# Kernel tuning notes

Hardware: AMD Instinct MI355X
Metric: run time of the kernel (lower is better)

The kernel has to match this reference:

```python
import jax, jax.numpy as jnp
import numpy as np

N = 100000   # nodes
E = 1000000  # edges
H = 64       # hidden_channels
METAPATH = (0, 1, 2)


def setup_inputs() -> dict:
    key = jax.random.key(0)
    ks = jax.random.split(key, 32)
    inp = {
        "x": jax.random.normal(ks[0], (N, 2 * H), dtype=jnp.float32),
        "edge_index": jax.random.randint(ks[1], (2, E), 0, N, dtype=jnp.int64),
        "edge_type": jax.random.randint(ks[2], (E,), 0, 3, dtype=jnp.int64),
    }
    # layer 0: in = 2H, layers 1,2: in = H; torch Linear weight is [out, in]
    ki = 3
    for l, in_dim in enumerate([2 * H, H, H]):
        for wname in ["wl", "w0", "w1"]:
            inp[f"{wname}{l}"] = jax.random.normal(ks[ki], (H, in_dim), dtype=jnp.float32) * 0.05
            ki += 1
            inp[f"{wname[0]}b{wname[1]}{l}"] = jnp.zeros((H,), dtype=jnp.float32)
    return inp


def _layer(x_in, h, mask, src, dst, wl, bl, w0, b0, w1, b1):
    # aggr='add', flow='target_to_source': agg[src[e]] += h[dst[e]] for masked edges
    msg = jnp.where(mask[:, None], h[dst], jnp.zeros((), h.dtype))  # [E, H]
    agg = jax.ops.segment_sum(msg, src, num_segments=N)             # [N, H]
    return agg @ wl.T + bl + h @ w0.T + b0 + x_in @ w1.T + b1


def reference(x, edge_index, edge_type,
              wl0, wbl0, w00, wb00, w10, wb10,
              wl1, wbl1, w01, wb01, w11, wb11,
              wl2, wbl2, w02, wb02, w12, wb12):
    src, dst = edge_index[0], edge_index[1]
    params = [
        (wl0, wbl0, w00, wb00, w10, wb10),
        (wl1, wbl1, w01, wb01, w11, wb11),
        (wl2, wbl2, w02, wb02, w12, wb12),
    ]
    h = x
    for i, rel in enumerate(METAPATH):
        mask = edge_type == rel
        x_in = x if i == 0 else h
        h = jax.nn.relu(_layer(x_in, h, mask, src, dst, *params[i]))
        # F.dropout with training=False is identity (eval mode reference)
    return h
```

## Files before the change

kernel.cpp:

```cpp
#include <hip/hip_runtime.h>
#include <cstdint>
#include <cstddef>

#define NNODES 100000
#define NEDGES 1000000
#define NREL 3
#define RN (NREL * NNODES)
#define EPB 2048
#define SCAN_BLOCKS ((RN + EPB - 1) / EPB)


__global__ __launch_bounds__(256) void hist_kernel(
    const int* __restrict__ srcv, const int* __restrict__ ety, int* __restrict__ cnt)
{
    const int e = (int)(blockIdx.x * 256 + threadIdx.x);
    if (e < NEDGES) atomicAdd(&cnt[ety[e] * NNODES + srcv[e]], 1);
}

__global__ __launch_bounds__(256) void scan_reduce(
    const int* __restrict__ cnt, int* __restrict__ bsum)
{
    __shared__ int sd[256];
    const int t = (int)threadIdx.x;
    const int base = (int)blockIdx.x * EPB + t * 8;
    int s = 0;
    #pragma unroll
    for (int i = 0; i < 8; ++i)
        if (base + i < RN) s += cnt[base + i];
    sd[t] = s;
    __syncthreads();
    for (int st = 128; st > 0; st >>= 1) {
        if (t < st) sd[t] += sd[t + st];
        __syncthreads();
    }
    if (t == 0) bsum[blockIdx.x] = sd[0];
}

__global__ __launch_bounds__(256) void scan_blocksums(int* __restrict__ bsum, int nb)
{
    __shared__ int buf0[256], buf1[256];
    const int t = (int)threadIdx.x;
    buf0[t] = (t < nb) ? bsum[t] : 0;
    __syncthreads();
    int* a = buf0; int* b = buf1;
    for (int st = 1; st < 256; st <<= 1) {
        int v = a[t];
        if (t >= st) v += a[t - st];
        b[t] = v;
        __syncthreads();
        int* tmp = a; a = b; b = tmp;
    }
    if (t < nb) bsum[t] = (t == 0) ? 0 : a[t - 1];
}

__global__ __launch_bounds__(256) void scan_final(
    const int* __restrict__ cnt, const int* __restrict__ bsum,
    int* __restrict__ off, int* __restrict__ wptr)
{
    __shared__ int buf0[256], buf1[256];
    const int t = (int)threadIdx.x;
    const int base = (int)blockIdx.x * EPB + t * 8;
    int v[8];
    int tot = 0;
    #pragma unroll
    for (int i = 0; i < 8; ++i) {
        v[i] = (base + i < RN) ? cnt[base + i] : 0;
        tot += v[i];
    }
    buf0[t] = tot;
    __syncthreads();
    int* a = buf0; int* b = buf1;
    for (int st = 1; st < 256; st <<= 1) {
        int s = a[t];
        if (t >= st) s += a[t - st];
        b[t] = s;
        __syncthreads();
        int* tmp = a; a = b; b = tmp;
    }
    int o = bsum[blockIdx.x] + ((t == 0) ? 0 : a[t - 1]);
    #pragma unroll
    for (int i = 0; i < 8; ++i) {
        if (base + i < RN) { off[base + i] = o; wptr[base + i] = o; }
        o += v[i];
    }
    if (blockIdx.x == 0 && t == 0) off[RN] = NEDGES;
}

__global__ __launch_bounds__(256) void fill_kernel(
    const int* __restrict__ srcv, const int* __restrict__ dstv,
    const int* __restrict__ ety, int* __restrict__ wptr, int* __restrict__ ebuf)
{
    const int e = (int)(blockIdx.x * 256 + threadIdx.x);
    if (e < NEDGES) {
        const int pos = atomicAdd(&wptr[ety[e] * NNODES + srcv[e]], 1);
        ebuf[pos] = dstv[e];
    }
}

template<int K>
__global__ __launch_bounds__(256) void fused_layer(
    const int* __restrict__ off, const int* __restrict__ ebuf,
    const float* __restrict__ h,
    const float* __restrict__ W1, const float* __restrict__ W2a, const float* __restrict__ W2b,
    const float* __restrict__ B1, const float* __restrict__ B2, const float* __restrict__ B3,
    float* __restrict__ out, int rel, int nNodes)
{
    constexpr int PAD = (K == 128) ? 132 : 68;
    __shared__ float Agg[64][PAD];
    __shared__ float As[16][64];
    __shared__ float Ws[16][64];

    const int t    = (int)threadIdx.x;
    const int lane = t & 63;
    const int wv   = t >> 6;
    const int n0   = (int)blockIdx.x * 64;

    const int* o = off + rel * NNODES;
    #pragma unroll 1
    for (int ii = 0; ii < 8; ++ii) {
        const int nlA = wv * 16 + ii;
        const int nlB = nlA + 8;
        const int nA = n0 + nlA, nB = n0 + nlB;
        int jA = 0, eA = 0, jB = 0, eB = 0;
        if (nA < nNodes) { jA = o[nA]; eA = o[nA + 1]; }
        if (nB < nNodes) { jB = o[nB]; eB = o[nB + 1]; }
        float a0A = 0.f, a1A = 0.f, a0B = 0.f, a1B = 0.f;
        while (jA < eA && jB < eB) {
            const int dA = ebuf[jA++];
            const int dB = ebuf[jB++];
            const float* hA = h + (size_t)dA * K;
            const float* hB = h + (size_t)dB * K;
            a0A += hA[lane]; a0B += hB[lane];
            if (K == 128) { a1A += hA[64 + lane]; a1B += hB[64 + lane]; }
        }
        while (jA < eA) {
            const float* hA = h + (size_t)ebuf[jA++] * K;
            a0A += hA[lane];
            if (K == 128) a1A += hA[64 + lane];
        }
        while (jB < eB) {
            const float* hB = h + (size_t)ebuf[jB++] * K;
            a0B += hB[lane];
            if (K == 128) a1B += hB[64 + lane];
        }
        Agg[nlA][lane] = a0A;
        Agg[nlB][lane] = a0B;
        if (K == 128) { Agg[nlA][64 + lane] = a1A; Agg[nlB][64 + lane] = a1B; }
    }
    __syncthreads();

    const int tx = t & 15;
    const int ty = t >> 4;
    const int srow = t >> 2;
    const int skk  = (t & 3) * 4;

    float4 acc[4];
    #pragma unroll
    for (int i = 0; i < 4; ++i) acc[i] = make_float4(0.f, 0.f, 0.f, 0.f);

    const int KC = K / 16;
    const int nA = n0 + srow;

    #pragma unroll 1
    for (int c = 0; c < KC; ++c) {
        const float4 wv4 = *(const float4*)(W1 + (size_t)srow * K + c * 16 + skk);
        __syncthreads();
        Ws[skk + 0][srow] = wv4.x; Ws[skk + 1][srow] = wv4.y;
        Ws[skk + 2][srow] = wv4.z; Ws[skk + 3][srow] = wv4.w;
        __syncthreads();
        #pragma unroll
        for (int k4 = 0; k4 < 4; ++k4) {
            const float4 w0 = *(const float4*)&Ws[k4 * 4 + 0][tx * 4];
            const float4 w1 = *(const float4*)&Ws[k4 * 4 + 1][tx * 4];
            const float4 w2 = *(const float4*)&Ws[k4 * 4 + 2][tx * 4];
            const float4 w3 = *(const float4*)&Ws[k4 * 4 + 3][tx * 4];
            #pragma unroll
            for (int i = 0; i < 4; ++i) {
                const float4 a4 = *(const float4*)&Agg[ty * 4 + i][c * 16 + k4 * 4];
                acc[i].x = fmaf(a4.x, w0.x, acc[i].x); acc[i].y = fmaf(a4.x, w0.y, acc[i].y);
                acc[i].z = fmaf(a4.x, w0.z, acc[i].z); acc[i].w = fmaf(a4.x, w0.w, acc[i].w);
                acc[i].x = fmaf(a4.y, w1.x, acc[i].x); acc[i].y = fmaf(a4.y, w1.y, acc[i].y);
                acc[i].z = fmaf(a4.y, w1.z, acc[i].z); acc[i].w = fmaf(a4.y, w1.w, acc[i].w);
                acc[i].x = fmaf(a4.z, w2.x, acc[i].x); acc[i].y = fmaf(a4.z, w2.y, acc[i].y);
                acc[i].z = fmaf(a4.z, w2.z, acc[i].z); acc[i].w = fmaf(a4.z, w2.w, acc[i].w);
                acc[i].x = fmaf(a4.w, w3.x, acc[i].x); acc[i].y = fmaf(a4.w, w3.y, acc[i].y);
                acc[i].z = fmaf(a4.w, w3.z, acc[i].z); acc[i].w = fmaf(a4.w, w3.w, acc[i].w);
            }
        }
    }

    #pragma unroll 1
    for (int c = 0; c < KC; ++c) {
        const int k0 = c * 16;
        float4 av = make_float4(0.f, 0.f, 0.f, 0.f);
        if (nA < nNodes) av = *(const float4*)(h + (size_t)nA * K + k0 + skk);
        const float4 a = *(const float4*)(W2a + (size_t)srow * K + k0 + skk);
        const float4 b = *(const float4*)(W2b + (size_t)srow * K + k0 + skk);
        const float4 wv4 = make_float4(a.x + b.x, a.y + b.y, a.z + b.z, a.w + b.w);

        __syncthreads();
        As[skk + 0][srow] = av.x; As[skk + 1][srow] = av.y;
        As[skk + 2][srow] = av.z; As[skk + 3][srow] = av.w;
        Ws[skk + 0][srow] = wv4.x; Ws[skk + 1][srow] = wv4.y;
        Ws[skk + 2][srow] = wv4.z; Ws[skk + 3][srow] = wv4.w;
        __syncthreads();

        #pragma unroll
        for (int k = 0; k < 16; ++k) {
            const float4 a4 = *(const float4*)&As[k][ty * 4];
            const float4 w4 = *(const float4*)&Ws[k][tx * 4];
            acc[0].x = fmaf(a4.x, w4.x, acc[0].x); acc[0].y = fmaf(a4.x, w4.y, acc[0].y);
            acc[0].z = fmaf(a4.x, w4.z, acc[0].z); acc[0].w = fmaf(a4.x, w4.w, acc[0].w);
            acc[1].x = fmaf(a4.y, w4.x, acc[1].x); acc[1].y = fmaf(a4.y, w4.y, acc[1].y);
            acc[1].z = fmaf(a4.y, w4.z, acc[1].z); acc[1].w = fmaf(a4.y, w4.w, acc[1].w);
            acc[2].x = fmaf(a4.z, w4.x, acc[2].x); acc[2].y = fmaf(a4.z, w4.y, acc[2].y);
            acc[2].z = fmaf(a4.z, w4.z, acc[2].z); acc[2].w = fmaf(a4.z, w4.w, acc[2].w);
            acc[3].x = fmaf(a4.w, w4.x, acc[3].x); acc[3].y = fmaf(a4.w, w4.y, acc[3].y);
            acc[3].z = fmaf(a4.w, w4.z, acc[3].z); acc[3].w = fmaf(a4.w, w4.w, acc[3].w);
        }
    }

    const float4 b1 = *(const float4*)(B1 + tx * 4);
    const float4 b2 = *(const float4*)(B2 + tx * 4);
    const float4 b3 = *(const float4*)(B3 + tx * 4);
    const float4 bias = make_float4(b1.x + b2.x + b3.x, b1.y + b2.y + b3.y,
                                    b1.z + b2.z + b3.z, b1.w + b2.w + b3.w);
    #pragma unroll
    for (int i = 0; i < 4; ++i) {
        const int n = n0 + ty * 4 + i;
        if (n < nNodes) {
            float4 r = make_float4(acc[i].x + bias.x, acc[i].y + bias.y,
                                   acc[i].z + bias.z, acc[i].w + bias.w);
            r.x = r.x > 0.f ? r.x : 0.f;
            r.y = r.y > 0.f ? r.y : 0.f;
            r.z = r.z > 0.f ? r.z : 0.f;
            r.w = r.w > 0.f ? r.w : 0.f;
            *(float4*)(out + (size_t)n * 64 + tx * 4) = r;
        }
    }
}

extern "C" void kernel_launch(void* const* d_in, const int* in_sizes, int n_in,
                              void* d_out, int out_size, void* d_ws, size_t ws_size,
                              hipStream_t stream)
{
    const float* x    = (const float*)d_in[0];
    const int*   eidx = (const int*)d_in[1];
    const int*   ety  = (const int*)d_in[2];
    const int*   srcv = eidx;
    const int*   dstv = eidx + NEDGES;

    const float* wl0 = (const float*)d_in[3];
    const float* bl0 = (const float*)d_in[4];
    const float* w00 = (const float*)d_in[5];
    const float* b00 = (const float*)d_in[6];
    const float* w10 = (const float*)d_in[7];
    const float* b10 = (const float*)d_in[8];

    const float* wl1 = (const float*)d_in[9];
    const float* bl1 = (const float*)d_in[10];
    const float* w01 = (const float*)d_in[11];
    const float* b01 = (const float*)d_in[12];
    const float* w11 = (const float*)d_in[13];
    const float* b11 = (const float*)d_in[14];

    const float* wl2 = (const float*)d_in[15];
    const float* bl2 = (const float*)d_in[16];
    const float* w02 = (const float*)d_in[17];
    const float* b02 = (const float*)d_in[18];
    const float* w12 = (const float*)d_in[19];
    const float* b12 = (const float*)d_in[20];

    char* p = (char*)d_ws;
    auto alloc = [&](size_t bytes) {
        char* r = p;
        p += (bytes + 255) & ~(size_t)255;
        return r;
    };
    int* cnt  = (int*)alloc((size_t)RN * 4);
    int* off  = (int*)alloc((size_t)(RN + 1) * 4);
    int* wptr = (int*)alloc((size_t)RN * 4);
    int* bsum = (int*)alloc(1024);
    int* ebuf = (int*)alloc((size_t)NEDGES * 4);
    float* h2 = (float*)alloc((size_t)NNODES * 64 * sizeof(float));
    float* h1 = (float*)d_out;

    const int edgeGrid  = (NEDGES + 255) / 256;
    const int fusedGrid = (NNODES + 63) / 64;

    hipMemsetAsync(cnt, 0, (size_t)RN * 4, stream);
    hist_kernel<<<edgeGrid, 256, 0, stream>>>(srcv, ety, cnt);
    scan_reduce<<<SCAN_BLOCKS, 256, 0, stream>>>(cnt, bsum);
    scan_blocksums<<<1, 256, 0, stream>>>(bsum, SCAN_BLOCKS);
    scan_final<<<SCAN_BLOCKS, 256, 0, stream>>>(cnt, bsum, off, wptr);
    fill_kernel<<<edgeGrid, 256, 0, stream>>>(srcv, dstv, ety, wptr, ebuf);

    fused_layer<128><<<fusedGrid, 256, 0, stream>>>(off, ebuf, x, wl0, w00, w10,
                                                    bl0, b00, b10, h1, 0, NNODES);
    fused_layer<64><<<fusedGrid, 256, 0, stream>>>(off, ebuf, h1, wl1, w01, w11,
                                                   bl1, b01, b11, h2, 1, NNODES);
    fused_layer<64><<<fusedGrid, 256, 0, stream>>>(off, ebuf, h2, wl2, w02, w12,
                                                   bl2, b02, b12, (float*)d_out, 2, NNODES);
}
```

Before: 520.5 us.

## Transform-before-aggregate: precompute bf16 Y=h·Wl and gather projected rows

Uses linearity, (sum h[dst]) Wl = sum (h[dst] Wl), to compute Y = h·Wl per node first and then gather Y rows per edge. Y is stored as packed bf16 so each gathered row is 128 bytes instead of 256/512 bytes of fp32. The next layer's Y is computed in the epilogue of the current layer from the tile held in shared memory. This shrinks random-gather traffic, which dominates the cost, at the price of bf16 rounding error in the aggregated messages, an extra GEMM kernel and extra Y buffers.

After: 503.6 us. -3.3%, faster.

```diff
diff --git a/kernel.cpp b/kernel.cpp
--- a/kernel.cpp
+++ b/kernel.cpp
@@ -8,6 +8,15 @@
 #define RN (NREL * NNODES)
 #define EPB 2048
 #define SCAN_BLOCKS ((RN + EPB - 1) / EPB)
+
+__device__ __forceinline__ uint32_t pack_bf2(float a, float b) {
+    uint32_t ua = __float_as_uint(a), ub = __float_as_uint(b);
+    ua = (ua + 0x7fffu + ((ua >> 16) & 1u)) >> 16;
+    ub = (ub + 0x7fffu + ((ub >> 16) & 1u)) >> 16;
+    return ua | (ub << 16);
+}
+__device__ __forceinline__ float bf_lo(uint32_t u) { return __uint_as_float(u << 16); }
+__device__ __forceinline__ float bf_hi(uint32_t u) { return __uint_as_float(u & 0xffff0000u); }
 
 
 __global__ __launch_bounds__(256) void hist_kernel(
@@ -98,105 +107,29 @@
 }
 
 template<int K>
-__global__ __launch_bounds__(256) void fused_layer(
-    const int* __restrict__ off, const int* __restrict__ ebuf,
-    const float* __restrict__ h,
-    const float* __restrict__ W1, const float* __restrict__ W2a, const float* __restrict__ W2b,
-    const float* __restrict__ B1, const float* __restrict__ B2, const float* __restrict__ B3,
-    float* __restrict__ out, int rel, int nNodes)
-{
-    constexpr int PAD = (K == 128) ? 132 : 68;
-    __shared__ float Agg[64][PAD];
+__global__ __launch_bounds__(256) void gemm_y(
+    const float* __restrict__ A, const float* __restrict__ W,
+    uint32_t* __restrict__ y, int nNodes)
+{
     __shared__ float As[16][64];
     __shared__ float Ws[16][64];
 
-    const int t    = (int)threadIdx.x;
-    const int lane = t & 63;
-    const int wv   = t >> 6;
-    const int n0   = (int)blockIdx.x * 64;
-
-    const int* o = off + rel * NNODES;
+    const int t  = (int)threadIdx.x;
+    const int tx = t & 15, ty = t >> 4;
+    const int n0 = (int)blockIdx.x * 64;
+    const int srow = t >> 2, skk = (t & 3) * 4;
+    const int nA = n0 + srow;
+
+    float4 acc[4];
+    #pragma unroll
+    for (int i = 0; i < 4; ++i) acc[i] = make_float4(0.f, 0.f, 0.f, 0.f);
+
     #pragma unroll 1
-    for (int ii = 0; ii < 8; ++ii) {
-        const int nlA = wv * 16 + ii;
-        const int nlB = nlA + 8;
-        const int nA = n0 + nlA, nB = n0 + nlB;
-        int jA = 0, eA = 0, jB = 0, eB = 0;
-        if (nA < nNodes) { jA = o[nA]; eA = o[nA + 1]; }
-        if (nB < nNodes) { jB = o[nB]; eB = o[nB + 1]; }
-        float a0A = 0.f, a1A = 0.f, a0B = 0.f, a1B = 0.f;
-        while (jA < eA && jB < eB) {
-            const int dA = ebuf[jA++];
-            const int dB = ebuf[jB++];
-            const float* hA = h + (size_t)dA * K;
-            const float* hB = h + (size_t)dB * K;
-            a0A += hA[lane]; a0B += hB[lane];
-            if (K == 128) { a1A += hA[64 + lane]; a1B += hB[64 + lane]; }
-        }
-        while (jA < eA) {
-            const float* hA = h + (size_t)ebuf[jA++] * K;
-            a0A += hA[lane];
-            if (K == 128) a1A += hA[64 + lane];
-        }
-        while (jB < eB) {
-            const float* hB = h + (size_t)ebuf[jB++] * K;
-            a0B += hB[lane];
-            if (K == 128) a1B += hB[64 + lane];
-        }
-        Agg[nlA][lane] = a0A;
-        Agg[nlB][lane] = a0B;
-        if (K == 128) { Agg[nlA][64 + lane] = a1A; Agg[nlB][64 + lane] = a1B; }
-    }
-    __syncthreads();
-
-    const int tx = t & 15;
-    const int ty = t >> 4;
-    const int srow = t >> 2;
-    const int skk  = (t & 3) * 4;
-
-    float4 acc[4];
-    #pragma unroll
-    for (int i = 0; i < 4; ++i) acc[i] = make_float4(0.f, 0.f, 0.f, 0.f);
-
-    const int KC = K / 16;
-    const int nA = n0 + srow;
-
-    #pragma unroll 1
-    for (int c = 0; c < KC; ++c) {
-        const float4 wv4 = *(const float4*)(W1 + (size_t)srow * K + c * 16 + skk);
-        __syncthreads();
-        Ws[skk + 0][srow] = wv4.x; Ws[skk + 1][srow] = wv4.y;
-        Ws[skk + 2][srow] = wv4.z; Ws[skk + 3][srow] = wv4.w;
-        __syncthreads();
-        #pragma unroll
-        for (int k4 = 0; k4 < 4; ++k4) {
-            const float4 w0 = *(const float4*)&Ws[k4 * 4 + 0][tx * 4];
-            const float4 w1 = *(const float4*)&Ws[k4 * 4 + 1][tx * 4];
-            const float4 w2 = *(const float4*)&Ws[k4 * 4 + 2][tx * 4];
-            const float4 w3 = *(const float4*)&Ws[k4 * 4 + 3][tx * 4];
-            #pragma unroll
-            for (int i = 0; i < 4; ++i) {
-                const float4 a4 = *(const float4*)&Agg[ty * 4 + i][c * 16 + k4 * 4];
-                acc[i].x = fmaf(a4.x, w0.x, acc[i].x); acc[i].y = fmaf(a4.x, w0.y, acc[i].y);
-                acc[i].z = fmaf(a4.x, w0.z, acc[i].z); acc[i].w = fmaf(a4.x, w0.w, acc[i].w);
-                acc[i].x = fmaf(a4.y, w1.x, acc[i].x); acc[i].y = fmaf(a4.y, w1.y, acc[i].y);
-                acc[i].z = fmaf(a4.y, w1.z, acc[i].z); acc[i].w = fmaf(a4.y, w1.w, acc[i].w);
-                acc[i].x = fmaf(a4.z, w2.x, acc[i].x); acc[i].y = fmaf(a4.z, w2.y, acc[i].y);
-                acc[i].z = fmaf(a4.z, w2.z, acc[i].z); acc[i].w = fmaf(a4.z, w2.w, acc[i].w);
-                acc[i].x = fmaf(a4.w, w3.x, acc[i].x); acc[i].y = fmaf(a4.w, w3.y, acc[i].y);
-                acc[i].z = fmaf(a4.w, w3.z, acc[i].z); acc[i].w = fmaf(a4.w, w3.w, acc[i].w);
-            }
-        }
-    }
-
-    #pragma unroll 1
-    for (int c = 0; c < KC; ++c) {
+    for (int c = 0; c < K / 16; ++c) {
         const int k0 = c * 16;
         float4 av = make_float4(0.f, 0.f, 0.f, 0.f);
-        if (nA < nNodes) av = *(const float4*)(h + (size_t)nA * K + k0 + skk);
-        const float4 a = *(const float4*)(W2a + (size_t)srow * K + k0 + skk);
-        const float4 b = *(const float4*)(W2b + (size_t)srow * K + k0 + skk);
-        const float4 wv4 = make_float4(a.x + b.x, a.y + b.y, a.z + b.z, a.w + b.w);
+        if (nA < nNodes) av = *(const float4*)(A + (size_t)nA * K + k0 + skk);
+        const float4 wv4 = *(const float4*)(W + (size_t)srow * K + k0 + skk);
 
         __syncthreads();
         As[skk + 0][srow] = av.x; As[skk + 1][srow] = av.y;
@@ -220,22 +153,147 @@
         }
     }
 
+    #pragma unroll
+    for (int i = 0; i < 4; ++i) {
+        const int n = n0 + ty * 4 + i;
+        if (n < nNodes) {
+            uint2 p;
+            p.x = pack_bf2(acc[i].x, acc[i].y);
+            p.y = pack_bf2(acc[i].z, acc[i].w);
+            *(uint2*)(y + (size_t)n * 32 + tx * 2) = p;
+        }
+    }
+}
+
+template<int K, bool HASY>
+__global__ __launch_bounds__(256) void dense_layer(
+    const float* __restrict__ h,
+    const uint32_t* __restrict__ ybuf,
+    const int* __restrict__ off, const int* __restrict__ ebuf, int rel,
+    const float* __restrict__ W2a, const float* __restrict__ W2b,
+    const float* __restrict__ B1, const float* __restrict__ B2, const float* __restrict__ B3,
+    const float* __restrict__ Wy,
+    float* __restrict__ out,
+    uint32_t* __restrict__ ynext,
+    int nNodes)
+{
+    __shared__ float As[16][64];
+    __shared__ float Ws[16][64];
+    __shared__ float Ot[HASY ? 64 : 1][76];
+
+    const int t  = (int)threadIdx.x;
+    const int tx = t & 15, ty = t >> 4;
+    const int n0 = (int)blockIdx.x * 64;
+    const int srow = t >> 2, skk = (t & 3) * 4;
+    const int nA = n0 + srow;
+
+    float4 acc[4];
+    #pragma unroll
+    for (int i = 0; i < 4; ++i) acc[i] = make_float4(0.f, 0.f, 0.f, 0.f);
+
+    #pragma unroll 1
+    for (int c = 0; c < K / 16; ++c) {
+        const int k0 = c * 16;
+        float4 av = make_float4(0.f, 0.f, 0.f, 0.f);
+        if (nA < nNodes) av = *(const float4*)(h + (size_t)nA * K + k0 + skk);
+        const float4 a = *(const float4*)(W2a + (size_t)srow * K + k0 + skk);
+        const float4 b = *(const float4*)(W2b + (size_t)srow * K + k0 + skk);
+        const float4 wv4 = make_float4(a.x + b.x, a.y + b.y, a.z + b.z, a.w + b.w);
+
+        __syncthreads();
+        As[skk + 0][srow] = av.x; As[skk + 1][srow] = av.y;
+        As[skk + 2][srow] = av.z; As[skk + 3][srow] = av.w;
+        Ws[skk + 0][srow] = wv4.x; Ws[skk + 1][srow] = wv4.y;
+        Ws[skk + 2][srow] = wv4.z; Ws[skk + 3][srow] = wv4.w;
+        __syncthreads();
+
+        #pragma unroll
+        for (int k = 0; k < 16; ++k) {
+            const float4 a4 = *(const float4*)&As[k][ty * 4];
+            const float4 w4 = *(const float4*)&Ws[k][tx * 4];
+            acc[0].x = fmaf(a4.x, w4.x, acc[0].x); acc[0].y = fmaf(a4.x, w4.y, acc[0].y);
+            acc[0].z = fmaf(a4.x, w4.z, acc[0].z); acc[0].w = fmaf(a4.x, w4.w, acc[0].w);
+            acc[1].x = fmaf(a4.y, w4.x, acc[1].x); acc[1].y = fmaf(a4.y, w4.y, acc[1].y);
+            acc[1].z = fmaf(a4.y, w4.z, acc[1].z); acc[1].w = fmaf(a4.y, w4.w, acc[1].w);
+            acc[2].x = fmaf(a4.z, w4.x, acc[2].x); acc[2].y = fmaf(a4.z, w4.y, acc[2].y);
+            acc[2].z = fmaf(a4.z, w4.z, acc[2].z); acc[2].w = fmaf(a4.z, w4.w, acc[2].w);
+            acc[3].x = fmaf(a4.w, w4.x, acc[3].x); acc[3].y = fmaf(a4.w, w4.y, acc[3].y);
+            acc[3].z = fmaf(a4.w, w4.z, acc[3].z); acc[3].w = fmaf(a4.w, w4.w, acc[3].w);
+        }
+    }
+
     const float4 b1 = *(const float4*)(B1 + tx * 4);
     const float4 b2 = *(const float4*)(B2 + tx * 4);
     const float4 b3 = *(const float4*)(B3 + tx * 4);
     const float4 bias = make_float4(b1.x + b2.x + b3.x, b1.y + b2.y + b3.y,
                                     b1.z + b2.z + b3.z, b1.w + b2.w + b3.w);
-    #pragma unroll
+    const int* o = off + rel * NNODES;
+
+    #pragma unroll 1
     for (int i = 0; i < 4; ++i) {
         const int n = n0 + ty * 4 + i;
+        float4 r = make_float4(acc[i].x + bias.x, acc[i].y + bias.y,
+                               acc[i].z + bias.z, acc[i].w + bias.w);
         if (n < nNodes) {
-            float4 r = make_float4(acc[i].x + bias.x, acc[i].y + bias.y,
-                                   acc[i].z + bias.z, acc[i].w + bias.w);
-            r.x = r.x > 0.f ? r.x : 0.f;
-            r.y = r.y > 0.f ? r.y : 0.f;
-            r.z = r.z > 0.f ? r.z : 0.f;
-            r.w = r.w > 0.f ? r.w : 0.f;
-            *(float4*)(out + (size_t)n * 64 + tx * 4) = r;
+            int j = o[n];
+            const int e1 = o[n + 1];
+            float4 g = make_float4(0.f, 0.f, 0.f, 0.f);
+            for (; j < e1; ++j) {
+                const uint2 v = *(const uint2*)(ybuf + (size_t)ebuf[j] * 32 + tx * 2);
+                g.x += bf_lo(v.x); g.y += bf_hi(v.x);
+                g.z += bf_lo(v.y); g.w += bf_hi(v.y);
+            }
+            r.x += g.x; r.y += g.y; r.z += g.z; r.w += g.w;
+        }
+        r.x = r.x > 0.f ? r.x : 0.f;
+        r.y = r.y > 0.f ? r.y : 0.f;
+        r.z = r.z > 0.f ? r.z : 0.f;
+        r.w = r.w > 0.f ? r.w : 0.f;
+        if (n < nNodes) *(float4*)(out + (size_t)n * 64 + tx * 4) = r;
+        if constexpr (HASY) *(float4*)&Ot[ty * 4 + i][tx * 4] = r;
+    }
+
+    if constexpr (HASY) {
+        float4 ya[4];
+        #pragma unroll
+        for (int i = 0; i < 4; ++i) ya[i] = make_float4(0.f, 0.f, 0.f, 0.f);
+
+        #pragma unroll 1
+        for (int c = 0; c < 4; ++c) {
+            const float4 wv4 = *(const float4*)(Wy + (size_t)srow * 64 + c * 16 + skk);
+            __syncthreads();
+            Ws[skk + 0][srow] = wv4.x; Ws[skk + 1][srow] = wv4.y;
+            Ws[skk + 2][srow] = wv4.z; Ws[skk + 3][srow] = wv4.w;
+            __syncthreads();
+            #pragma unroll
+            for (int k4 = 0; k4 < 4; ++k4) {
+                const float4 w0 = *(const float4*)&Ws[k4 * 4 + 0][tx * 4];
+                const float4 w1 = *(const float4*)&Ws[k4 * 4 + 1][tx * 4];
+                const float4 w2 = *(const float4*)&Ws[k4 * 4 + 2][tx * 4];
+                const float4 w3 = *(const float4*)&Ws[k4 * 4 + 3][tx * 4];
+                #pragma unroll
+                for (int i = 0; i < 4; ++i) {
+                    const float4 a4 = *(const float4*)&Ot[ty * 4 + i][c * 16 + k4 * 4];
+                    ya[i].x = fmaf(a4.x, w0.x, ya[i].x); ya[i].y = fmaf(a4.x, w0.y, ya[i].y);
+                    ya[i].z = fmaf(a4.x, w0.z, ya[i].z); ya[i].w = fmaf(a4.x, w0.w, ya[i].w);
+                    ya[i].x = fmaf(a4.y, w1.x, ya[i].x); ya[i].y = fmaf(a4.y, w1.y, ya[i].y);
+                    ya[i].z = fmaf(a4.y, w1.z, ya[i].z); ya[i].w = fmaf(a4.y, w1.w, ya[i].w);
+                    ya[i].x = fmaf(a4.z, w2.x, ya[i].x); ya[i].y = fmaf(a4.z, w2.y, ya[i].y);
+                    ya[i].z = fmaf(a4.z, w2.z, ya[i].z); ya[i].w = fmaf(a4.z, w2.w, ya[i].w);
+                    ya[i].x = fmaf(a4.w, w3.x, ya[i].x); ya[i].y = fmaf(a4.w, w3.y, ya[i].y);
+                    ya[i].z = fmaf(a4.w, w3.z, ya[i].z); ya[i].w = fmaf(a4.w, w3.w, ya[i].w);
+                }
+            }
+        }
+        #pragma unroll
+        for (int i = 0; i < 4; ++i) {
+            const int n = n0 + ty * 4 + i;
+            if (n < nNodes) {
+                uint2 p;
+                p.x = pack_bf2(ya[i].x, ya[i].y);
+                p.y = pack_bf2(ya[i].z, ya[i].w);
+                *(uint2*)(ynext + (size_t)n * 32 + tx * 2) = p;
+            }
         }
     }
 }
@@ -282,11 +340,13 @@
     int* wptr = (int*)alloc((size_t)RN * 4);
     int* bsum = (int*)alloc(1024);
     int* ebuf = (int*)alloc((size_t)NEDGES * 4);
-    float* h2 = (float*)alloc((size_t)NNODES * 64 * sizeof(float));
-    float* h1 = (float*)d_out;
+    uint32_t* yA = (uint32_t*)alloc((size_t)NNODES * 32 * 4);
+    uint32_t* yB = (uint32_t*)alloc((size_t)NNODES * 32 * 4);
+    float* h2    = (float*)alloc((size_t)NNODES * 64 * sizeof(float));
+    float* h1    = (float*)d_out;
 
     const int edgeGrid  = (NEDGES + 255) / 256;
-    const int fusedGrid = (NNODES + 63) / 64;
+    const int tileGrid  = (NNODES + 63) / 64;
 
     hipMemsetAsync(cnt, 0, (size_t)RN * 4, stream);
     hist_kernel<<<edgeGrid, 256, 0, stream>>>(srcv, ety, cnt);
@@ -295,10 +355,15 @@
     scan_final<<<SCAN_BLOCKS, 256, 0, stream>>>(cnt, bsum, off, wptr);
     fill_kernel<<<edgeGrid, 256, 0, stream>>>(srcv, dstv, ety, wptr, ebuf);
 
-    fused_layer<128><<<fusedGrid, 256, 0, stream>>>(off, ebuf, x, wl0, w00, w10,
-                                                    bl0, b00, b10, h1, 0, NNODES);
-    fused_layer<64><<<fusedGrid, 256, 0, stream>>>(off, ebuf, h1, wl1, w01, w11,
-                                                   bl1, b01, b11, h2, 1, NNODES);
-    fused_layer<64><<<fusedGrid, 256, 0, stream>>>(off, ebuf, h2, wl2, w02, w12,
-                                                   bl2, b02, b12, (float*)d_out, 2, NNODES);
-}
+    gemm_y<128><<<tileGrid, 256, 0, stream>>>(x, wl0, yA, NNODES);
+
+    dense_layer<128, true><<<tileGrid, 256, 0, stream>>>(
+        x, yA, off, ebuf, 0, w00, w10, bl0, b00, b10, wl1, h1, yB, NNODES);
+
+    dense_layer<64, true><<<tileGrid, 256, 0, stream>>>(
+        h1, yB, off, ebuf, 1, w01, w11, bl1, b01, b11, wl2, h2, yA, NNODES);
+
+    dense_layer<64, false><<<tileGrid, 256, 0, stream>>>(
+        h2, yA, off, ebuf, 2, w02, w12, bl2, b02, b12, nullptr,
+        (float*)d_out, nullptr, NNODES);
+}
```
